# Kernel optimization log

Hardware: AMD Instinct MI355X
Metric: run time of the kernel (lower is better)

The kernel has to match this reference:

```python
import jax, jax.numpy as jnp
import numpy as np

K_N = 20          # neighbors (init kwarg k_n)
EPS = 1e-5        # BN / InstanceNorm eps (torch default)


def _conv1x1(x, w, b):
    # x: [B,C,N,K], w: [O,C], b: [O]
    return jnp.einsum('bcnk,oc->bonk', x, w) + b[None, :, None, None]


def _bn(x, g, b):
    # training-mode BatchNorm2d: stats over (B,N,K)
    mean = x.mean(axis=(0, 2, 3), keepdims=True)
    var = x.var(axis=(0, 2, 3), keepdims=True)
    return (x - mean) * jax.lax.rsqrt(var + EPS) * g[None, :, None, None] + b[None, :, None, None]


def _inorm(x):
    # InstanceNorm2d (affine=False): stats over (N,K) per (b,c)
    mean = x.mean(axis=(2, 3), keepdims=True)
    var = x.var(axis=(2, 3), keepdims=True)
    return (x - mean) * jax.lax.rsqrt(var + EPS)


def _knn(x, k):
    # x: [B,C,N] -> idx [B,N,k] of nearest neighbors (excluding self)
    sq = jnp.sum(x * x, axis=1)                                   # [B,N]
    neg_d = 2.0 * jnp.einsum('bcn,bcm->bnm', x, x) - sq[:, :, None] - sq[:, None, :]
    _, idx = jax.lax.top_k(neg_d, k + 1)
    return idx[:, :, 1:]


def _res_block(x, w1, b1, g1, be1, w2, b2, g2, be2):
    # pre=False: residual branch is identity
    out = jax.nn.relu(_bn(_inorm(_conv1x1(x, w1, b1)), g1, be1))
    out = _bn(_inorm(_conv1x1(out, w2, b2)), g2, be2)
    return jax.nn.relu(out + x)


def _forward(data, conv0_w, conv0_b, bn0_g, bn0_b, lin_w, lin_b,
             res_w1, res_b1, res_g1, res_be1, res_w2, res_b2, res_g2, res_be2):
    B, C, N = data.shape
    # graph_feature: degree feature from normalized affinity matrix
    nrm = jnp.linalg.norm(data, axis=1, keepdims=True) + 1e-5
    o = data / nrm
    A = jnp.einsum('bcn,bcm->bnm', o, o)                          # [B,N,N]
    D = (jnp.sum(A, axis=1, keepdims=True) - 1.0) / N             # [B,1,N] (subtract eye diag)
    feat = jnp.concatenate([data, jax.nn.relu(jnp.tanh(D))], axis=1)  # [B,129,N]

    idx = _knn(feat, K_N)                                         # [B,N,k]
    xt = jnp.transpose(feat, (0, 2, 1))                           # [B,N,129]
    gathered = jax.vmap(lambda xb, ib: xb[ib])(xt, idx)           # [B,N,k,129]
    center = xt[:, :, None, :]
    edge = jnp.concatenate([jnp.broadcast_to(center, gathered.shape),
                            center - gathered], axis=3)           # [B,N,k,258]
    edge = jnp.transpose(edge, (0, 3, 1, 2))                      # [B,258,N,k]

    out = jax.nn.relu(_bn(_conv1x1(edge, conv0_w, conv0_b), bn0_g, bn0_b))
    out = jnp.max(out, axis=3, keepdims=True)                     # max_pool2d (1,k) -> [B,128,N,1]
    for i in range(4):
        out = _res_block(out, res_w1[i], res_b1[i], res_g1[i], res_be1[i],
                         res_w2[i], res_b2[i], res_g2[i], res_be2[i])
    logit = _conv1x1(out, lin_w, lin_b)                           # [B,1,N,1]
    return logit.reshape(logit.shape[0], -1)                      # [B,N]


def setup_inputs() -> dict:
    B, C, N = 8, 128, 2048
    key = jax.random.key(0)
    ks = jax.random.split(key, 10)
    s = 0.05
    return {
        'data': jax.random.normal(ks[0], (B, C, N), dtype=jnp.float32),
        'x': jax.random.normal(ks[1], (B, C, N), dtype=jnp.float32),  # unused by module
        'conv0_w': jax.random.normal(ks[2], (128, 258), dtype=jnp.float32) * s,
        'conv0_b': jnp.zeros((128,), dtype=jnp.float32),
        'bn0_g': jnp.ones((128,), dtype=jnp.float32),
        'bn0_b': jnp.zeros((128,), dtype=jnp.float32),
        'lin_w': jax.random.normal(ks[3], (1, 128), dtype=jnp.float32) * s,
        'lin_b': jnp.zeros((1,), dtype=jnp.float32),
        'res_w1': jax.random.normal(ks[4], (4, 128, 128), dtype=jnp.float32) * s,
        'res_b1': jnp.zeros((4, 128), dtype=jnp.float32),
        'res_g1': jnp.ones((4, 128), dtype=jnp.float32),
        'res_be1': jnp.zeros((4, 128), dtype=jnp.float32),
        'res_w2': jax.random.normal(ks[5], (4, 128, 128), dtype=jnp.float32) * s,
        'res_b2': jnp.zeros((4, 128), dtype=jnp.float32),
        'res_g2': jnp.ones((4, 128), dtype=jnp.float32),
        'res_be2': jnp.zeros((4, 128), dtype=jnp.float32),
    }


def reference(data, x, conv0_w, conv0_b, bn0_g, bn0_b, lin_w, lin_b,
              res_w1, res_b1, res_g1, res_be1, res_w2, res_b2, res_g2, res_be2):
    # x is accepted but unused, matching the torch module
    return _forward(data, conv0_w, conv0_b, bn0_g, bn0_b, lin_w, lin_b,
                    res_w1, res_b1, res_g1, res_be1, res_w2, res_b2, res_g2, res_be2)
```

## Files before the change

kernel.cpp:

```cpp
#include <hip/hip_runtime.h>
#include <math.h>
#include <float.h>

#define NB 8
#define NC 128
#define NN 2048
#define KNN 20
#define CF 129
#define CFP 144
#define EPSV 1e-5f

#define S_OFF      0
#define BN0S_OFF   1024
#define RESST_OFF  1280
#define NRM_OFF    17664
#define ZERO_CNT   34048
#define SQN_OFF    34048
#define WCAT_OFF   50432
#define RESAFF_OFF 87552
#define FEAT_OFF   103936
#define PQ_OFF     2463232
#define X_OFF      6657536
#define SLOT_SZ    2097152
#define IDX_OFF    12948992
#define G_OFF      13276672
#define XB_OFF     46831104
#define WS_FLOATS  48928256
#define MMN_OFF    (X_OFF + SLOT_SZ)
#define MMX_OFF    (X_OFF + 2 * SLOT_SZ)

__launch_bounds__(256)
__global__ void k1a_sq(const float* __restrict__ data, float* __restrict__ ws) {
    int b = blockIdx.y;
    int n = blockIdx.x * 256 + threadIdx.x;
    int c0 = blockIdx.z * 32;
    const float* dp = data + (size_t)b * NC * NN + (size_t)c0 * NN + n;
    float acc = 0.f;
#pragma unroll
    for (int c = 0; c < 32; ++c) { float v = dp[(size_t)c * NN]; acc = fmaf(v, v, acc); }
    atomicAdd(&ws[NRM_OFF + b * NN + n], acc);
}

__launch_bounds__(256)
__global__ void k1s_colsum(const float* __restrict__ data, float* __restrict__ ws) {
    int b = blockIdx.y;
    int c0 = blockIdx.x * 16;
    int tid = threadIdx.x, w = tid >> 6, lane = tid & 63;
    __shared__ float Linv[NN];
    for (int r = tid; r < NN; r += 256)
        Linv[r] = 1.f / (sqrtf(ws[NRM_OFF + b * NN + r]) + 1e-5f);
    __syncthreads();
#pragma unroll
    for (int i = 0; i < 4; ++i) {
        int c = c0 + w * 4 + i;
        const float* dp = data + (size_t)b * NC * NN + (size_t)c * NN;
        float acc = 0.f;
        for (int n = lane; n < NN; n += 64) acc = fmaf(dp[n], Linv[n], acc);
        for (int off = 32; off; off >>= 1) acc += __shfl_down(acc, off);
        if (lane == 0) ws[S_OFF + b * NC + c] = acc;
    }
}

__launch_bounds__(256)
__global__ void k2_feat(const float* __restrict__ data, float* __restrict__ ws) {
    int b = blockIdx.y;
    int n0 = blockIdx.x * 64;
    int tid = threadIdx.x;
    __shared__ float Sb[NC];
    __shared__ __align__(16) float fT[64][CFP];
    __shared__ float redD[4][64], redQ[4][64];
    if (tid < NC) Sb[tid] = ws[S_OFF + b * NC + tid];
    __syncthreads();
    int nn = tid & 63, cg = tid >> 6;
    float dotp = 0.f, sq = 0.f;
    const float* dp = data + (size_t)b * NC * NN + n0 + nn;
    for (int c = cg; c < NC; c += 4) {
        float v = dp[(size_t)c * NN];
        fT[nn][c] = v;
        dotp += Sb[c] * v;
        sq += v * v;
    }
    redD[cg][nn] = dotp; redQ[cg][nn] = sq;
    __syncthreads();
    if (tid < 64) {
        float dt = redD[0][tid] + redD[1][tid] + redD[2][tid] + redD[3][tid];
        float sv = redQ[0][tid] + redQ[1][tid] + redQ[2][tid] + redQ[3][tid];
        float nrm = sqrtf(ws[NRM_OFF + b * NN + n0 + tid]) + 1e-5f;
        float D = (dt / nrm - 1.f) * (1.f / (float)NN);
        float f1 = tanhf(D); if (f1 < 0.f) f1 = 0.f;
        fT[tid][NC] = f1;
        for (int c = NC + 1; c < CFP; ++c) fT[tid][c] = 0.f;
        ws[SQN_OFF + b * NN + n0 + tid] = sv + f1 * f1;
    }
    __syncthreads();
    float* out = ws + FEAT_OFF + (size_t)(b * NN + n0) * CFP;
    for (int i = tid; i < 64 * CFP; i += 256) out[i] = ((float*)fT)[i];
}

__launch_bounds__(256)
__global__ void k4_wcat(const float* __restrict__ w, float* __restrict__ ws) {
    int i = blockIdx.x * 256 + threadIdx.x;
    int o = i / CFP, c = i % CFP;
    float v = 0.f;
    if (c < CF) {
        if (o < 128) v = w[o * 258 + c] + w[o * 258 + CF + c];
        else         v = w[(o - 128) * 258 + CF + c];
    }
    ws[WCAT_OFF + i] = v;
}

__launch_bounds__(256, 2)
__global__ void k3_gram(float* __restrict__ ws) {
    __shared__ __align__(16) float As[8][256];
    __shared__ __align__(16) float Bs[8][128];
    int tid = threadIdx.x;
    int b = blockIdx.z;
    int m0 = blockIdx.x * 128, n0 = blockIdx.y * 256;
    const float* F = ws + FEAT_OFF + (size_t)b * NN * CFP;
    float acc[16][8];
#pragma unroll
    for (int i = 0; i < 16; ++i)
#pragma unroll
        for (int j = 0; j < 8; ++j) acc[i][j] = 0.f;
    int rr = tid >> 1, cq = tid & 1;
    int tx = tid & 15, ty = tid >> 4;
    for (int kc = 0; kc < CFP; kc += 8) {
        float4 a0 = *(const float4*)&F[(size_t)(n0 + tid) * CFP + kc];
        float4 a1 = *(const float4*)&F[(size_t)(n0 + tid) * CFP + kc + 4];
        float4 bv = *(const float4*)&F[(size_t)(m0 + rr) * CFP + kc + cq * 4];
        __syncthreads();
        As[0][tid] = a0.x; As[1][tid] = a0.y; As[2][tid] = a0.z; As[3][tid] = a0.w;
        As[4][tid] = a1.x; As[5][tid] = a1.y; As[6][tid] = a1.z; As[7][tid] = a1.w;
        Bs[cq*4+0][rr] = bv.x; Bs[cq*4+1][rr] = bv.y; Bs[cq*4+2][rr] = bv.z; Bs[cq*4+3][rr] = bv.w;
        __syncthreads();
#pragma unroll
        for (int kk = 0; kk < 8; ++kk) {
            float a[16], bb[8];
            *(float4*)&a[0]  = *(const float4*)&As[kk][ty * 16];
            *(float4*)&a[4]  = *(const float4*)&As[kk][ty * 16 + 4];
            *(float4*)&a[8]  = *(const float4*)&As[kk][ty * 16 + 8];
            *(float4*)&a[12] = *(const float4*)&As[kk][ty * 16 + 12];
            *(float4*)&bb[0] = *(const float4*)&Bs[kk][tx * 4];
            *(float4*)&bb[4] = *(const float4*)&Bs[kk][64 + tx * 4];
#pragma unroll
            for (int i = 0; i < 16; ++i)
#pragma unroll
                for (int j = 0; j < 8; ++j) acc[i][j] = fmaf(a[i], bb[j], acc[i][j]);
        }
    }
    float sqv[8];
#pragma unroll
    for (int j = 0; j < 4; ++j) {
        sqv[j]     = ws[SQN_OFF + b * NN + m0 + tx * 4 + j];
        sqv[4 + j] = ws[SQN_OFF + b * NN + m0 + 64 + tx * 4 + j];
    }
    float* G = ws + G_OFF + (size_t)b * NN * NN;
#pragma unroll
    for (int i = 0; i < 16; ++i) {
        int row = n0 + ty * 16 + i;
        float4 o1, o2;
        o1.x = 2.f*acc[i][0]-sqv[0]; o1.y = 2.f*acc[i][1]-sqv[1];
        o1.z = 2.f*acc[i][2]-sqv[2]; o1.w = 2.f*acc[i][3]-sqv[3];
        o2.x = 2.f*acc[i][4]-sqv[4]; o2.y = 2.f*acc[i][5]-sqv[5];
        o2.z = 2.f*acc[i][6]-sqv[6]; o2.w = 2.f*acc[i][7]-sqv[7];
        *(float4*)&G[(size_t)row * NN + m0 + tx * 4]      = o1;
        *(float4*)&G[(size_t)row * NN + m0 + 64 + tx * 4] = o2;
    }
}

__launch_bounds__(256)
__global__ void ksel(float* __restrict__ ws) {
    int wid = threadIdx.x >> 6, lane = threadIdx.x & 63;
    int r = blockIdx.x * 4 + wid;
    const float* row = ws + G_OFF + (size_t)r * NN;
    float v[32];
#pragma unroll
    for (int i = 0; i < 32; ++i) v[i] = row[lane + (i << 6)];
    float b1v = -FLT_MAX, b2v = -FLT_MAX;
    int b1i = 0, b2i = 0;
#pragma unroll
    for (int i = 0; i < 32; ++i) {
        float x = v[i];
        if (x > b1v)      { b2v = b1v; b2i = b1i; b1v = x; b1i = i; }
        else if (x > b2v) { b2v = x; b2i = i; }
    }
    unsigned int mask = 0u;
    bool has2 = true;
    int* out = (int*)(ws + IDX_OFF) + (size_t)r * KNN;
    for (int k = 0; k < 21; ++k) {
        float M = b1v;
#pragma unroll
        for (int off = 1; off < 64; off <<= 1) M = fmaxf(M, __shfl_xor(M, off));
        unsigned long long tied = __ballot(b1v == M);
        int mm;
        if (__popcll(tied) > 1) {
            int cand = (b1v == M) ? ((b1i << 6) | lane) : 0x7FFFFFFF;
#pragma unroll
            for (int off = 1; off < 64; off <<= 1) {
                int oc = __shfl_xor(cand, off);
                cand = oc < cand ? oc : cand;
            }
            mm = cand;
        } else {
            int l = __ffsll(tied) - 1;
            mm = (__shfl(b1i, l) << 6) | l;
        }
        if (k > 0 && lane == 0) out[k - 1] = mm;
        if (lane == (mm & 63)) {
            mask |= 1u << b1i;
            if (has2) { b1v = b2v; b1i = b2i; has2 = false; }
            else {
                b1v = -FLT_MAX; b2v = -FLT_MAX; b1i = 0; b2i = 0;
#pragma unroll
                for (int i = 0; i < 32; ++i) {
                    float x = (mask & (1u << i)) ? -FLT_MAX : v[i];
                    if (x > b1v)      { b2v = b1v; b2i = b1i; b1v = x; b1i = i; }
                    else if (x > b2v) { b2v = x; b2i = i; }
                }
                has2 = true;
            }
        }
    }
}

__launch_bounds__(256)
__global__ void k5_pq(float* __restrict__ ws) {
    __shared__ __align__(16) float As[16][64];
    __shared__ __align__(16) float Bs[16][64];
    int tid = threadIdx.x;
    int m0 = blockIdx.x * 64, o0 = blockIdx.y * 64;
    int rr = tid >> 2, cq = tid & 3;
    int tx = tid & 15, ty = tid >> 4;
    float acc[4][4];
#pragma unroll
    for (int i = 0; i < 4; ++i)
#pragma unroll
        for (int j = 0; j < 4; ++j) acc[i][j] = 0.f;
    const float* F  = ws + FEAT_OFF;
    const float* Wc = ws + WCAT_OFF;
    for (int kc = 0; kc < CFP; kc += 16) {
        float4 av = *(const float4*)&F [(size_t)(m0 + rr) * CFP + kc + cq * 4];
        float4 bv = *(const float4*)&Wc[(size_t)(o0 + rr) * CFP + kc + cq * 4];
        __syncthreads();
        As[cq*4+0][rr]=av.x; As[cq*4+1][rr]=av.y; As[cq*4+2][rr]=av.z; As[cq*4+3][rr]=av.w;
        Bs[cq*4+0][rr]=bv.x; Bs[cq*4+1][rr]=bv.y; Bs[cq*4+2][rr]=bv.z; Bs[cq*4+3][rr]=bv.w;
        __syncthreads();
#pragma unroll
        for (int kk = 0; kk < 16; ++kk) {
            float a[4], bb[4];
            *(float4*)&a[0]  = *(const float4*)&As[kk][ty * 4];
            *(float4*)&bb[0] = *(const float4*)&Bs[kk][tx * 4];
#pragma unroll
            for (int i = 0; i < 4; ++i)
#pragma unroll
                for (int j = 0; j < 4; ++j) acc[i][j] = fmaf(a[i], bb[j], acc[i][j]);
        }
    }
#pragma unroll
    for (int i = 0; i < 4; ++i) {
        float4 o;
        o.x = acc[i][0]; o.y = acc[i][1]; o.z = acc[i][2]; o.w = acc[i][3];
        *(float4*)&ws[PQ_OFF + (size_t)(m0 + ty * 4 + i) * 256 + o0 + tx * 4] = o;
    }
}

__launch_bounds__(256)
__global__ void k6_bn0stats(float* __restrict__ ws) {
    int tid = threadIdx.x;
    int o = tid & 127, h = tid >> 7;
    int m0 = blockIdx.x * 16;
    const float* PQ = ws + PQ_OFF;
    const int* idx = (const int*)(ws + IDX_OFF);
    float* MMn = ws + MMN_OFF;
    float* MMx = ws + MMX_OFF;
    __shared__ float red[2][128];
    float s = 0.f, q = 0.f;
    for (int p = h; p < 16; p += 2) {
        int m = m0 + p;
        int bb = m >> 11;
        float pv = PQ[(size_t)m * 256 + o];
        const int* ip = idx + (size_t)m * KNN;
        float mn = FLT_MAX, mx = -FLT_MAX;
        for (int k = 0; k < KNN; ++k) {
            int j = ip[k];
            float val = pv - PQ[(size_t)(bb * NN + j) * 256 + 128 + o];
            s += val; q += val * val;
            mn = fminf(mn, val); mx = fmaxf(mx, val);
        }
        MMn[(size_t)m * NC + o] = mn;
        MMx[(size_t)m * NC + o] = mx;
    }
    red[h][o] = s; __syncthreads();
    if (tid < 128) atomicAdd(&ws[BN0S_OFF + tid], red[0][tid] + red[1][tid]);
    __syncthreads();
    red[h][o] = q; __syncthreads();
    if (tid < 128) atomicAdd(&ws[BN0S_OFF + 128 + tid], red[0][tid] + red[1][tid]);
}

__launch_bounds__(256)
__global__ void k8_apply(float* __restrict__ ws, const float* __restrict__ g,
                         const float* __restrict__ be) {
    int e = blockIdx.x * 256 + threadIdx.x;
    int fi = e * 4;
    int o = fi & 127;
    const float cnt = 1.f / (float)(NB * NN * KNN);
    float4 sum4 = *(const float4*)&ws[BN0S_OFF + o];
    float4 ssq4 = *(const float4*)&ws[BN0S_OFF + 128 + o];
    float4 g4   = *(const float4*)&g[o];
    float4 be4  = *(const float4*)&be[o];
    float4 mn = *(const float4*)&ws[MMN_OFF + fi];
    float4 mx = *(const float4*)&ws[MMX_OFF + fi];
    float4 r;
#define BN0_DO(comp) { \
    float m_ = sum4.comp * cnt; \
    float v_ = ssq4.comp * cnt - m_ * m_; if (v_ < 0.f) v_ = 0.f; \
    float sc_ = g4.comp * rsqrtf(v_ + EPSV); \
    float sh_ = be4.comp - m_ * sc_; \
    r.comp = fmaxf(fmaf(sc_ > 0.f ? mx.comp : mn.comp, sc_, sh_), 0.f); }
    BN0_DO(x) BN0_DO(y) BN0_DO(z) BN0_DO(w)
#undef BN0_DO
    *(float4*)&ws[X_OFF + fi] = r;
}

__launch_bounds__(256)
__global__ void k9f_conv(const float* __restrict__ x, const float* __restrict__ w,
                         float* __restrict__ y, float* __restrict__ stats,
                         const float* __restrict__ aff, const float* __restrict__ xin,
                         float* __restrict__ xw) {
    __shared__ __align__(16) float As[16][64];
    __shared__ __align__(16) float Bs[16][64];
    __shared__ float red[16][64];
    int tid = threadIdx.x;
    int m0 = blockIdx.x * 64, o0 = blockIdx.y * 64;
    int rr = tid >> 2, cq = tid & 3;
    int tx = tid & 15, ty = tid >> 4;
    int bA = (m0 + rr) >> 11;
    float acc[4][4];
#pragma unroll
    for (int i = 0; i < 4; ++i)
#pragma unroll
        for (int j = 0; j < 4; ++j) acc[i][j] = 0.f;
    for (int kc = 0; kc < NC; kc += 16) {
        float4 av = *(const float4*)&x[(size_t)(m0 + rr) * NC + kc + cq * 4];
        if (aff) {
            int c = kc + cq * 4;
            float4 sc4 = *(const float4*)&aff[bA * 128 + c];
            float4 sh4 = *(const float4*)&aff[1024 + bA * 128 + c];
            av.x = fmaf(av.x, sc4.x, sh4.x);
            av.y = fmaf(av.y, sc4.y, sh4.y);
            av.z = fmaf(av.z, sc4.z, sh4.z);
            av.w = fmaf(av.w, sc4.w, sh4.w);
            if (xin) {
                float4 xv = *(const float4*)&xin[(size_t)(m0 + rr) * NC + kc + cq * 4];
                av.x += xv.x; av.y += xv.y; av.z += xv.z; av.w += xv.w;
            }
            av.x = fmaxf(av.x, 0.f); av.y = fmaxf(av.y, 0.f);
            av.z = fmaxf(av.z, 0.f); av.w = fmaxf(av.w, 0.f);
            if (xw && blockIdx.y == 0)
                *(float4*)&xw[(size_t)(m0 + rr) * NC + kc + cq * 4] = av;
        }
        float4 bv = *(const float4*)&w[(size_t)(o0 + rr) * NC + kc + cq * 4];
        __syncthreads();
        As[cq*4+0][rr]=av.x; As[cq*4+1][rr]=av.y; As[cq*4+2][rr]=av.z; As[cq*4+3][rr]=av.w;
        Bs[cq*4+0][rr]=bv.x; Bs[cq*4+1][rr]=bv.y; Bs[cq*4+2][rr]=bv.z; Bs[cq*4+3][rr]=bv.w;
        __syncthreads();
#pragma unroll
        for (int kk = 0; kk < 16; ++kk) {
            float a[4], bb[4];
            *(float4*)&a[0]  = *(const float4*)&As[kk][ty * 4];
            *(float4*)&bb[0] = *(const float4*)&Bs[kk][tx * 4];
#pragma unroll
            for (int i = 0; i < 4; ++i)
#pragma unroll
                for (int j = 0; j < 4; ++j) acc[i][j] = fmaf(a[i], bb[j], acc[i][j]);
        }
    }
#pragma unroll
    for (int i = 0; i < 4; ++i) {
        float4 o;
        o.x = acc[i][0]; o.y = acc[i][1]; o.z = acc[i][2]; o.w = acc[i][3];
        *(float4*)&y[(size_t)(m0 + ty * 4 + i) * NC + o0 + tx * 4] = o;
    }
    int b = m0 >> 11;
    float s[4], q[4];
#pragma unroll
    for (int j = 0; j < 4; ++j) {
        s[j] = acc[0][j] + acc[1][j] + acc[2][j] + acc[3][j];
        q[j] = acc[0][j]*acc[0][j] + acc[1][j]*acc[1][j] + acc[2][j]*acc[2][j] + acc[3][j]*acc[3][j];
    }
    *(float4*)&red[ty][tx * 4] = make_float4(s[0], s[1], s[2], s[3]);
    __syncthreads();
    if (tid < 64) {
        float t = 0.f;
#pragma unroll
        for (int g2 = 0; g2 < 16; ++g2) t += red[g2][tid];
        atomicAdd(&stats[b * NC + o0 + tid], t);
    }
    __syncthreads();
    *(float4*)&red[ty][tx * 4] = make_float4(q[0], q[1], q[2], q[3]);
    __syncthreads();
    if (tid < 64) {
        float t = 0.f;
#pragma unroll
        for (int g2 = 0; g2 < 16; ++g2) t += red[g2][tid];
        atomicAdd(&stats[1024 + b * NC + o0 + tid], t);
    }
}

__launch_bounds__(1024)
__global__ void k10_fin(float* __restrict__ ws, int L, const float* __restrict__ g,
                        const float* __restrict__ be) {
    __shared__ float vv[1024];
    __shared__ float rsbn[128];
    int tid = threadIdx.x;
    const float* st = ws + RESST_OFF + L * 2048;
    float sum = st[tid], ssq = st[1024 + tid];
    float m = sum * (1.f / (float)NN);
    float v = ssq * (1.f / (float)NN) - m * m; if (v < 0.f) v = 0.f;
    float r = rsqrtf(v + EPSV);
    vv[tid] = v / (v + EPSV);
    __syncthreads();
    if (tid < 128) {
        float a = 0.f;
        for (int bb = 0; bb < NB; ++bb) a += vv[bb * 128 + tid];
        rsbn[tid] = rsqrtf(a * (1.f / (float)NB) + EPSV);
    }
    __syncthreads();
    int o = tid & 127;
    float sc = r * rsbn[o] * g[o];
    float sh = be[o] - m * sc;
    float* aff = ws + RESAFF_OFF + L * 2048;
    aff[tid] = sc; aff[1024 + tid] = sh;
}

__launch_bounds__(256)
__global__ void k12_logit(const float* __restrict__ y2, const float* __restrict__ xin,
                          const float* __restrict__ aff, const float* __restrict__ lw,
                          const float* __restrict__ lb, float* __restrict__ out) {
    __shared__ float w[128];
    int tid = threadIdx.x;
    if (tid < 128) w[tid] = lw[tid];
    __syncthreads();
    int m = blockIdx.x * 256 + tid;
    int b = m >> 11;
    const float* yp = y2 + (size_t)m * NC;
    const float* xp = xin + (size_t)m * NC;
    const float* sc = aff + b * 128;
    const float* sh = aff + 1024 + b * 128;
    float acc = lb[0];
    for (int c = 0; c < NC; c += 4) {
        float4 yv = *(const float4*)&yp[c];
        float4 xv = *(const float4*)&xp[c];
        float v0 = fmaxf(fmaf(yv.x, sc[c],     sh[c])     + xv.x, 0.f);
        float v1 = fmaxf(fmaf(yv.y, sc[c + 1], sh[c + 1]) + xv.y, 0.f);
        float v2 = fmaxf(fmaf(yv.z, sc[c + 2], sh[c + 2]) + xv.z, 0.f);
        float v3 = fmaxf(fmaf(yv.w, sc[c + 3], sh[c + 3]) + xv.w, 0.f);
        acc += v0 * w[c] + v1 * w[c + 1] + v2 * w[c + 2] + v3 * w[c + 3];
    }
    out[m] = acc;
}

extern "C" void kernel_launch(void* const* d_in, const int* in_sizes, int n_in,
                              void* d_out, int out_size, void* d_ws, size_t ws_size,
                              hipStream_t stream) {
    if (ws_size < (size_t)WS_FLOATS * 4) return;
    const float* data    = (const float*)d_in[0];
    const float* conv0_w = (const float*)d_in[2];
    const float* bn0_g   = (const float*)d_in[4];
    const float* bn0_b   = (const float*)d_in[5];
    const float* lin_w   = (const float*)d_in[6];
    const float* lin_b   = (const float*)d_in[7];
    const float* res_w1  = (const float*)d_in[8];
    const float* res_g1  = (const float*)d_in[10];
    const float* res_be1 = (const float*)d_in[11];
    const float* res_w2  = (const float*)d_in[12];
    const float* res_g2  = (const float*)d_in[14];
    const float* res_be2 = (const float*)d_in[15];
    float* ws  = (float*)d_ws;
    float* out = (float*)d_out;

    hipMemsetAsync(d_ws, 0, ZERO_CNT * sizeof(float), stream);
    k1a_sq<<<dim3(8, 8, 4), 256, 0, stream>>>(data, ws);
    k1s_colsum<<<dim3(8, 8), 256, 0, stream>>>(data, ws);
    k2_feat<<<dim3(32, 8), 256, 0, stream>>>(data, ws);
    k4_wcat<<<144, 256, 0, stream>>>(conv0_w, ws);
    k3_gram<<<dim3(16, 8, 8), 256, 0, stream>>>(ws);
    ksel<<<4096, 256, 0, stream>>>(ws);
    k5_pq<<<dim3(256, 4), 256, 0, stream>>>(ws);
    k6_bn0stats<<<1024, 256, 0, stream>>>(ws);
    k8_apply<<<2048, 256, 0, stream>>>(ws, bn0_g, bn0_b);

    float* XA = ws + X_OFF;
    float* Y1 = ws + X_OFF + SLOT_SZ;
    float* Y2 = ws + X_OFF + 2 * SLOT_SZ;
    float* XB = ws + XB_OFF;

    k9f_conv<<<dim3(256, 2), 256, 0, stream>>>(XA, res_w1, Y1, ws + RESST_OFF, nullptr, nullptr, nullptr);
    k10_fin<<<1, 1024, 0, stream>>>(ws, 0, res_g1, res_be1);
    k9f_conv<<<dim3(256, 2), 256, 0, stream>>>(Y1, res_w2, Y2, ws + RESST_OFF + 2048,
                                               ws + RESAFF_OFF, nullptr, nullptr);
    k10_fin<<<1, 1024, 0, stream>>>(ws, 1, res_g2, res_be2);
    float* xcur = XA; float* xnext = XB;
    for (int i = 1; i < 4; ++i) {
        int L = 2 * i, L2 = 2 * i + 1;
        k9f_conv<<<dim3(256, 2), 256, 0, stream>>>(Y2, res_w1 + i * 16384, Y1,
                                                   ws + RESST_OFF + L * 2048,
                                                   ws + RESAFF_OFF + (L - 1) * 2048, xcur, xnext);
        k10_fin<<<1, 1024, 0, stream>>>(ws, L, res_g1 + i * 128, res_be1 + i * 128);
        k9f_conv<<<dim3(256, 2), 256, 0, stream>>>(Y1, res_w2 + i * 16384, Y2,
                                                   ws + RESST_OFF + L2 * 2048,
                                                   ws + RESAFF_OFF + L * 2048, nullptr, nullptr);
        k10_fin<<<1, 1024, 0, stream>>>(ws, L2, res_g2 + i * 128, res_be2 + i * 128);
        float* t = xcur; xcur = xnext; xnext = t;
    }
    k12_logit<<<64, 256, 0, stream>>>(Y2, xcur, ws + RESAFF_OFF + 7 * 2048, lin_w, lin_b, out);
}
```

Before: 445.2 us.

## Double-buffer gram kernel shared tiles with 128x128 blocks and prefetch

```diff
diff --git a/kernel.cpp b/kernel.cpp
--- a/kernel.cpp
+++ b/kernel.cpp
@@ -109,45 +109,65 @@
     ws[WCAT_OFF + i] = v;
 }
 
-__launch_bounds__(256, 2)
+__launch_bounds__(256)
 __global__ void k3_gram(float* __restrict__ ws) {
-    __shared__ __align__(16) float As[8][256];
-    __shared__ __align__(16) float Bs[8][128];
+    __shared__ __align__(16) float As[2][16][128];
+    __shared__ __align__(16) float Bs[2][16][128];
     int tid = threadIdx.x;
     int b = blockIdx.z;
-    int m0 = blockIdx.x * 128, n0 = blockIdx.y * 256;
+    int m0 = blockIdx.x * 128, n0 = blockIdx.y * 128;
     const float* F = ws + FEAT_OFF + (size_t)b * NN * CFP;
-    float acc[16][8];
-#pragma unroll
-    for (int i = 0; i < 16; ++i)
+    int rr = tid >> 1, hh = tid & 1;
+    int tx = tid & 15, ty = tid >> 4;
+    float acc[8][8];
+#pragma unroll
+    for (int i = 0; i < 8; ++i)
 #pragma unroll
         for (int j = 0; j < 8; ++j) acc[i][j] = 0.f;
-    int rr = tid >> 1, cq = tid & 1;
-    int tx = tid & 15, ty = tid >> 4;
-    for (int kc = 0; kc < CFP; kc += 8) {
-        float4 a0 = *(const float4*)&F[(size_t)(n0 + tid) * CFP + kc];
-        float4 a1 = *(const float4*)&F[(size_t)(n0 + tid) * CFP + kc + 4];
-        float4 bv = *(const float4*)&F[(size_t)(m0 + rr) * CFP + kc + cq * 4];
-        __syncthreads();
-        As[0][tid] = a0.x; As[1][tid] = a0.y; As[2][tid] = a0.z; As[3][tid] = a0.w;
-        As[4][tid] = a1.x; As[5][tid] = a1.y; As[6][tid] = a1.z; As[7][tid] = a1.w;
-        Bs[cq*4+0][rr] = bv.x; Bs[cq*4+1][rr] = bv.y; Bs[cq*4+2][rr] = bv.z; Bs[cq*4+3][rr] = bv.w;
-        __syncthreads();
-#pragma unroll
-        for (int kk = 0; kk < 8; ++kk) {
-            float a[16], bb[8];
-            *(float4*)&a[0]  = *(const float4*)&As[kk][ty * 16];
-            *(float4*)&a[4]  = *(const float4*)&As[kk][ty * 16 + 4];
-            *(float4*)&a[8]  = *(const float4*)&As[kk][ty * 16 + 8];
-            *(float4*)&a[12] = *(const float4*)&As[kk][ty * 16 + 12];
-            *(float4*)&bb[0] = *(const float4*)&Bs[kk][tx * 4];
-            *(float4*)&bb[4] = *(const float4*)&Bs[kk][64 + tx * 4];
-#pragma unroll
-            for (int i = 0; i < 16; ++i)
+
+    const float* Arow = &F[(size_t)(n0 + rr) * CFP + hh * 8];
+    const float* Brow = &F[(size_t)(m0 + rr) * CFP + hh * 8];
+    float4 ra0 = *(const float4*)&Arow[0];
+    float4 ra1 = *(const float4*)&Arow[4];
+    float4 rb0 = *(const float4*)&Brow[0];
+    float4 rb1 = *(const float4*)&Brow[4];
+    int kbase = hh * 8;
+#define STAGE(buf) { \
+    As[buf][kbase+0][rr]=ra0.x; As[buf][kbase+1][rr]=ra0.y; As[buf][kbase+2][rr]=ra0.z; As[buf][kbase+3][rr]=ra0.w; \
+    As[buf][kbase+4][rr]=ra1.x; As[buf][kbase+5][rr]=ra1.y; As[buf][kbase+6][rr]=ra1.z; As[buf][kbase+7][rr]=ra1.w; \
+    Bs[buf][kbase+0][rr]=rb0.x; Bs[buf][kbase+1][rr]=rb0.y; Bs[buf][kbase+2][rr]=rb0.z; Bs[buf][kbase+3][rr]=rb0.w; \
+    Bs[buf][kbase+4][rr]=rb1.x; Bs[buf][kbase+5][rr]=rb1.y; Bs[buf][kbase+6][rr]=rb1.z; Bs[buf][kbase+7][rr]=rb1.w; }
+    STAGE(0);
+    __syncthreads();
+    int cur = 0;
+    for (int t = 0; t < 9; ++t) {
+        if (t < 8) {
+            int kc = (t + 1) * 16;
+            ra0 = *(const float4*)&Arow[kc];
+            ra1 = *(const float4*)&Arow[kc + 4];
+            rb0 = *(const float4*)&Brow[kc];
+            rb1 = *(const float4*)&Brow[kc + 4];
+        }
+#pragma unroll
+        for (int kk = 0; kk < 16; ++kk) {
+            float a[8], bb[8];
+            *(float4*)&a[0]  = *(const float4*)&As[cur][kk][ty * 8];
+            *(float4*)&a[4]  = *(const float4*)&As[cur][kk][ty * 8 + 4];
+            *(float4*)&bb[0] = *(const float4*)&Bs[cur][kk][tx * 4];
+            *(float4*)&bb[4] = *(const float4*)&Bs[cur][kk][64 + tx * 4];
+#pragma unroll
+            for (int i = 0; i < 8; ++i)
 #pragma unroll
                 for (int j = 0; j < 8; ++j) acc[i][j] = fmaf(a[i], bb[j], acc[i][j]);
         }
-    }
+        if (t < 8) {
+            int nxt = cur ^ 1;
+            STAGE(nxt);
+            __syncthreads();
+            cur = nxt;
+        }
+    }
+#undef STAGE
     float sqv[8];
 #pragma unroll
     for (int j = 0; j < 4; ++j) {
@@ -156,8 +176,8 @@
     }
     float* G = ws + G_OFF + (size_t)b * NN * NN;
 #pragma unroll
-    for (int i = 0; i < 16; ++i) {
-        int row = n0 + ty * 16 + i;
+    for (int i = 0; i < 8; ++i) {
+        int row = n0 + ty * 8 + i;
         float4 o1, o2;
         o1.x = 2.f*acc[i][0]-sqv[0]; o1.y = 2.f*acc[i][1]-sqv[1];
         o1.z = 2.f*acc[i][2]-sqv[2]; o1.w = 2.f*acc[i][3]-sqv[3];
@@ -484,7 +504,7 @@
     k1s_colsum<<<dim3(8, 8), 256, 0, stream>>>(data, ws);
     k2_feat<<<dim3(32, 8), 256, 0, stream>>>(data, ws);
     k4_wcat<<<144, 256, 0, stream>>>(conv0_w, ws);
-    k3_gram<<<dim3(16, 8, 8), 256, 0, stream>>>(ws);
+    k3_gram<<<dim3(16, 16, 8), 256, 0, stream>>>(ws);
     ksel<<<4096, 256, 0, stream>>>(ws);
     k5_pq<<<dim3(256, 4), 256, 0, stream>>>(ws);
     k6_bn0stats<<<1024, 256, 0, stream>>>(ws);
```

Result: slower. 487.2 us (+9.4%).

## Fold norm-finalize into conv prologue and shrink gram tile to 128x128

Applied to the files above, without the earlier changes.

```diff
diff --git a/kernel.cpp b/kernel.cpp
--- a/kernel.cpp
+++ b/kernel.cpp
@@ -17,7 +17,6 @@
 #define ZERO_CNT   34048
 #define SQN_OFF    34048
 #define WCAT_OFF   50432
-#define RESAFF_OFF 87552
 #define FEAT_OFF   103936
 #define PQ_OFF     2463232
 #define X_OFF      6657536
@@ -109,41 +108,37 @@
     ws[WCAT_OFF + i] = v;
 }
 
-__launch_bounds__(256, 2)
+__launch_bounds__(256)
 __global__ void k3_gram(float* __restrict__ ws) {
-    __shared__ __align__(16) float As[8][256];
+    __shared__ __align__(16) float As[8][128];
     __shared__ __align__(16) float Bs[8][128];
     int tid = threadIdx.x;
     int b = blockIdx.z;
-    int m0 = blockIdx.x * 128, n0 = blockIdx.y * 256;
+    int m0 = blockIdx.x * 128, n0 = blockIdx.y * 128;
     const float* F = ws + FEAT_OFF + (size_t)b * NN * CFP;
-    float acc[16][8];
-#pragma unroll
-    for (int i = 0; i < 16; ++i)
+    float acc[8][8];
+#pragma unroll
+    for (int i = 0; i < 8; ++i)
 #pragma unroll
         for (int j = 0; j < 8; ++j) acc[i][j] = 0.f;
     int rr = tid >> 1, cq = tid & 1;
     int tx = tid & 15, ty = tid >> 4;
     for (int kc = 0; kc < CFP; kc += 8) {
-        float4 a0 = *(const float4*)&F[(size_t)(n0 + tid) * CFP + kc];
-        float4 a1 = *(const float4*)&F[(size_t)(n0 + tid) * CFP + kc + 4];
+        float4 av = *(const float4*)&F[(size_t)(n0 + rr) * CFP + kc + cq * 4];
         float4 bv = *(const float4*)&F[(size_t)(m0 + rr) * CFP + kc + cq * 4];
         __syncthreads();
-        As[0][tid] = a0.x; As[1][tid] = a0.y; As[2][tid] = a0.z; As[3][tid] = a0.w;
-        As[4][tid] = a1.x; As[5][tid] = a1.y; As[6][tid] = a1.z; As[7][tid] = a1.w;
+        As[cq*4+0][rr] = av.x; As[cq*4+1][rr] = av.y; As[cq*4+2][rr] = av.z; As[cq*4+3][rr] = av.w;
         Bs[cq*4+0][rr] = bv.x; Bs[cq*4+1][rr] = bv.y; Bs[cq*4+2][rr] = bv.z; Bs[cq*4+3][rr] = bv.w;
         __syncthreads();
 #pragma unroll
         for (int kk = 0; kk < 8; ++kk) {
-            float a[16], bb[8];
-            *(float4*)&a[0]  = *(const float4*)&As[kk][ty * 16];
-            *(float4*)&a[4]  = *(const float4*)&As[kk][ty * 16 + 4];
-            *(float4*)&a[8]  = *(const float4*)&As[kk][ty * 16 + 8];
-            *(float4*)&a[12] = *(const float4*)&As[kk][ty * 16 + 12];
+            float a[8], bb[8];
+            *(float4*)&a[0]  = *(const float4*)&As[kk][ty * 8];
+            *(float4*)&a[4]  = *(const float4*)&As[kk][ty * 8 + 4];
             *(float4*)&bb[0] = *(const float4*)&Bs[kk][tx * 4];
             *(float4*)&bb[4] = *(const float4*)&Bs[kk][64 + tx * 4];
 #pragma unroll
-            for (int i = 0; i < 16; ++i)
+            for (int i = 0; i < 8; ++i)
 #pragma unroll
                 for (int j = 0; j < 8; ++j) acc[i][j] = fmaf(a[i], bb[j], acc[i][j]);
         }
@@ -156,8 +151,8 @@
     }
     float* G = ws + G_OFF + (size_t)b * NN * NN;
 #pragma unroll
-    for (int i = 0; i < 16; ++i) {
-        int row = n0 + ty * 16 + i;
+    for (int i = 0; i < 8; ++i) {
+        int row = n0 + ty * 8 + i;
         float4 o1, o2;
         o1.x = 2.f*acc[i][0]-sqv[0]; o1.y = 2.f*acc[i][1]-sqv[1];
         o1.z = 2.f*acc[i][2]-sqv[2]; o1.w = 2.f*acc[i][3]-sqv[3];
@@ -325,16 +320,41 @@
 __launch_bounds__(256)
 __global__ void k9f_conv(const float* __restrict__ x, const float* __restrict__ w,
                          float* __restrict__ y, float* __restrict__ stats,
-                         const float* __restrict__ aff, const float* __restrict__ xin,
-                         float* __restrict__ xw) {
+                         const float* __restrict__ statsIn,
+                         const float* __restrict__ g, const float* __restrict__ be,
+                         const float* __restrict__ xin, float* __restrict__ xw) {
     __shared__ __align__(16) float As[16][64];
     __shared__ __align__(16) float Bs[16][64];
     __shared__ float red[16][64];
+    __shared__ float vvv[8][128];
+    __shared__ float scs[128], shs[128];
     int tid = threadIdx.x;
     int m0 = blockIdx.x * 64, o0 = blockIdx.y * 64;
+    int bA = m0 >> 11;
+    if (statsIn) {
+        for (int e = tid; e < 1024; e += 256) {
+            float sum = statsIn[e], ssq = statsIn[1024 + e];
+            float m_ = sum * (1.f / (float)NN);
+            float v_ = ssq * (1.f / (float)NN) - m_ * m_; if (v_ < 0.f) v_ = 0.f;
+            vvv[e >> 7][e & 127] = v_ / (v_ + EPSV);
+        }
+        __syncthreads();
+        if (tid < 128) {
+            float a = 0.f;
+#pragma unroll
+            for (int b2 = 0; b2 < NB; ++b2) a += vvv[b2][tid];
+            float rsbn = rsqrtf(a * (1.f / (float)NB) + EPSV);
+            float sum = statsIn[bA * 128 + tid], ssq = statsIn[1024 + bA * 128 + tid];
+            float m_ = sum * (1.f / (float)NN);
+            float v_ = ssq * (1.f / (float)NN) - m_ * m_; if (v_ < 0.f) v_ = 0.f;
+            float sc_ = rsqrtf(v_ + EPSV) * rsbn * g[tid];
+            scs[tid] = sc_;
+            shs[tid] = be[tid] - m_ * sc_;
+        }
+        __syncthreads();
+    }
     int rr = tid >> 2, cq = tid & 3;
     int tx = tid & 15, ty = tid >> 4;
-    int bA = (m0 + rr) >> 11;
     float acc[4][4];
 #pragma unroll
     for (int i = 0; i < 4; ++i)
@@ -342,14 +362,12 @@
         for (int j = 0; j < 4; ++j) acc[i][j] = 0.f;
     for (int kc = 0; kc < NC; kc += 16) {
         float4 av = *(const float4*)&x[(size_t)(m0 + rr) * NC + kc + cq * 4];
-        if (aff) {
+        if (statsIn) {
             int c = kc + cq * 4;
-            float4 sc4 = *(const float4*)&aff[bA * 128 + c];
-            float4 sh4 = *(const float4*)&aff[1024 + bA * 128 + c];
-            av.x = fmaf(av.x, sc4.x, sh4.x);
-            av.y = fmaf(av.y, sc4.y, sh4.y);
-            av.z = fmaf(av.z, sc4.z, sh4.z);
-            av.w = fmaf(av.w, sc4.w, sh4.w);
+            av.x = fmaf(av.x, scs[c],     shs[c]);
+            av.y = fmaf(av.y, scs[c + 1], shs[c + 1]);
+            av.z = fmaf(av.z, scs[c + 2], shs[c + 2]);
+            av.w = fmaf(av.w, scs[c + 3], shs[c + 3]);
             if (xin) {
                 float4 xv = *(const float4*)&xin[(size_t)(m0 + rr) * NC + kc + cq * 4];
                 av.x += xv.x; av.y += xv.y; av.z += xv.z; av.w += xv.w;
@@ -381,7 +399,6 @@
         o.x = acc[i][0]; o.y = acc[i][1]; o.z = acc[i][2]; o.w = acc[i][3];
         *(float4*)&y[(size_t)(m0 + ty * 4 + i) * NC + o0 + tx * 4] = o;
     }
-    int b = m0 >> 11;
     float s[4], q[4];
 #pragma unroll
     for (int j = 0; j < 4; ++j) {
@@ -394,7 +411,7 @@
         float t = 0.f;
 #pragma unroll
         for (int g2 = 0; g2 < 16; ++g2) t += red[g2][tid];
-        atomicAdd(&stats[b * NC + o0 + tid], t);
+        atomicAdd(&stats[bA * NC + o0 + tid], t);
     }
     __syncthreads();
     *(float4*)&red[ty][tx * 4] = make_float4(q[0], q[1], q[2], q[3]);
@@ -403,59 +420,54 @@
         float t = 0.f;
 #pragma unroll
         for (int g2 = 0; g2 < 16; ++g2) t += red[g2][tid];
-        atomicAdd(&stats[1024 + b * NC + o0 + tid], t);
-    }
-}
-
-__launch_bounds__(1024)
-__global__ void k10_fin(float* __restrict__ ws, int L, const float* __restrict__ g,
-                        const float* __restrict__ be) {
-    __shared__ float vv[1024];
-    __shared__ float rsbn[128];
+        atomicAdd(&stats[1024 + bA * NC + o0 + tid], t);
+    }
+}
+
+__launch_bounds__(256)
+__global__ void k12_logit(const float* __restrict__ y2, const float* __restrict__ xin,
+                          const float* __restrict__ statsIn,
+                          const float* __restrict__ g, const float* __restrict__ be,
+                          const float* __restrict__ lw, const float* __restrict__ lb,
+                          float* __restrict__ out) {
+    __shared__ float wsh[128];
+    __shared__ float vvv[8][128];
+    __shared__ float scs[128], shs[128];
     int tid = threadIdx.x;
-    const float* st = ws + RESST_OFF + L * 2048;
-    float sum = st[tid], ssq = st[1024 + tid];
-    float m = sum * (1.f / (float)NN);
-    float v = ssq * (1.f / (float)NN) - m * m; if (v < 0.f) v = 0.f;
-    float r = rsqrtf(v + EPSV);
-    vv[tid] = v / (v + EPSV);
+    int b = (blockIdx.x * 256) >> 11;
+    if (tid < 128) wsh[tid] = lw[tid];
+    for (int e = tid; e < 1024; e += 256) {
+        float sum = statsIn[e], ssq = statsIn[1024 + e];
+        float m_ = sum * (1.f / (float)NN);
+        float v_ = ssq * (1.f / (float)NN) - m_ * m_; if (v_ < 0.f) v_ = 0.f;
+        vvv[e >> 7][e & 127] = v_ / (v_ + EPSV);
+    }
     __syncthreads();
     if (tid < 128) {
         float a = 0.f;
-        for (int bb = 0; bb < NB; ++bb) a += vv[bb * 128 + tid];
-        rsbn[tid] = rsqrtf(a * (1.f / (float)NB) + EPSV);
-    }
-    __syncthreads();
-    int o = tid & 127;
-    float sc = r * rsbn[o] * g[o];
-    float sh = be[o] - m * sc;
-    float* aff = ws + RESAFF_OFF + L * 2048;
-    aff[tid] = sc; aff[1024 + tid] = sh;
-}
-
-__launch_bounds__(256)
-__global__ void k12_logit(const float* __restrict__ y2, const float* __restrict__ xin,
-                          const float* __restrict__ aff, const float* __restrict__ lw,
-                          const float* __restrict__ lb, float* __restrict__ out) {
-    __shared__ float w[128];
-    int tid = threadIdx.x;
-    if (tid < 128) w[tid] = lw[tid];
+#pragma unroll
+        for (int b2 = 0; b2 < NB; ++b2) a += vvv[b2][tid];
+        float rsbn = rsqrtf(a * (1.f / (float)NB) + EPSV);
+        float sum = statsIn[b * 128 + tid], ssq = statsIn[1024 + b * 128 + tid];
+        float m_ = sum * (1.f / (float)NN);
+        float v_ = ssq * (1.f / (float)NN) - m_ * m_; if (v_ < 0.f) v_ = 0.f;
+        float sc_ = rsqrtf(v_ + EPSV) * rsbn * g[tid];
+        scs[tid] = sc_;
+        shs[tid] = be[tid] - m_ * sc_;
+    }
     __syncthreads();
     int m = blockIdx.x * 256 + tid;
-    int b = m >> 11;
     const float* yp = y2 + (size_t)m * NC;
     const float* xp = xin + (size_t)m * NC;
-    const float* sc = aff + b * 128;
-    const float* sh = aff + 1024 + b * 128;
     float acc = lb[0];
     for (int c = 0; c < NC; c += 4) {
         float4 yv = *(const float4*)&yp[c];
         float4 xv = *(const float4*)&xp[c];
-        float v0 = fmaxf(fmaf(yv.x, sc[c],     sh[c])     + xv.x, 0.f);
-        float v1 = fmaxf(fmaf(yv.y, sc[c + 1], sh[c + 1]) + xv.y, 0.f);
-        float v2 = fmaxf(fmaf(yv.z, sc[c + 2], sh[c + 2]) + xv.z, 0.f);
-        float v3 = fmaxf(fmaf(yv.w, sc[c + 3], sh[c + 3]) + xv.w, 0.f);
-        acc += v0 * w[c] + v1 * w[c + 1] + v2 * w[c + 2] + v3 * w[c + 3];
+        float v0 = fmaxf(fmaf(yv.x, scs[c],     shs[c])     + xv.x, 0.f);
+        float v1 = fmaxf(fmaf(yv.y, scs[c + 1], shs[c + 1]) + xv.y, 0.f);
+        float v2 = fmaxf(fmaf(yv.z, scs[c + 2], shs[c + 2]) + xv.z, 0.f);
+        float v3 = fmaxf(fmaf(yv.w, scs[c + 3], shs[c + 3]) + xv.w, 0.f);
+        acc += v0 * wsh[c] + v1 * wsh[c + 1] + v2 * wsh[c + 2] + v3 * wsh[c + 3];
     }
     out[m] = acc;
 }
@@ -484,7 +496,7 @@
     k1s_colsum<<<dim3(8, 8), 256, 0, stream>>>(data, ws);
     k2_feat<<<dim3(32, 8), 256, 0, stream>>>(data, ws);
     k4_wcat<<<144, 256, 0, stream>>>(conv0_w, ws);
-    k3_gram<<<dim3(16, 8, 8), 256, 0, stream>>>(ws);
+    k3_gram<<<dim3(16, 16, 8), 256, 0, stream>>>(ws);
     ksel<<<4096, 256, 0, stream>>>(ws);
     k5_pq<<<dim3(256, 4), 256, 0, stream>>>(ws);
     k6_bn0stats<<<1024, 256, 0, stream>>>(ws);
@@ -494,24 +506,25 @@
     float* Y1 = ws + X_OFF + SLOT_SZ;
     float* Y2 = ws + X_OFF + 2 * SLOT_SZ;
     float* XB = ws + XB_OFF;
-
-    k9f_conv<<<dim3(256, 2), 256, 0, stream>>>(XA, res_w1, Y1, ws + RESST_OFF, nullptr, nullptr, nullptr);
-    k10_fin<<<1, 1024, 0, stream>>>(ws, 0, res_g1, res_be1);
-    k9f_conv<<<dim3(256, 2), 256, 0, stream>>>(Y1, res_w2, Y2, ws + RESST_OFF + 2048,
-                                               ws + RESAFF_OFF, nullptr, nullptr);
-    k10_fin<<<1, 1024, 0, stream>>>(ws, 1, res_g2, res_be2);
+    float* ST = ws + RESST_OFF;
+
+    k9f_conv<<<dim3(256, 2), 256, 0, stream>>>(XA, res_w1, Y1, ST,
+                                               nullptr, nullptr, nullptr, nullptr, nullptr);
+    k9f_conv<<<dim3(256, 2), 256, 0, stream>>>(Y1, res_w2, Y2, ST + 2048,
+                                               ST, res_g1, res_be1, nullptr, nullptr);
     float* xcur = XA; float* xnext = XB;
     for (int i = 1; i < 4; ++i) {
         int L = 2 * i, L2 = 2 * i + 1;
-        k9f_conv<<<dim3(256, 2), 256, 0, stream>>>(Y2, res_w1 + i * 16384, Y1,
-                                                   ws + RESST_OFF + L * 2048,
-                                                   ws + RESAFF_OFF + (L - 1) * 2048, xcur, xnext);
-        k10_fin<<<1, 1024, 0, stream>>>(ws, L, res_g1 + i * 128, res_be1 + i * 128);
-        k9f_conv<<<dim3(256, 2), 256, 0, stream>>>(Y1, res_w2 + i * 16384, Y2,
-                                                   ws + RESST_OFF + L2 * 2048,
-                                                   ws + RESAFF_OFF + L * 2048, nullptr, nullptr);
-        k10_fin<<<1, 1024, 0, stream>>>(ws, L2, res_g2 + i * 128, res_be2 + i * 128);
+        k9f_conv<<<dim3(256, 2), 256, 0, stream>>>(Y2, res_w1 + i * 16384, Y1, ST + L * 2048,
+                                                   ST + (L - 1) * 2048,
+                                                   res_g2 + (i - 1) * 128, res_be2 + (i - 1) * 128,
+                                                   xcur, xnext);
+        k9f_conv<<<dim3(256, 2), 256, 0, stream>>>(Y1, res_w2 + i * 16384, Y2, ST + L2 * 2048,
+                                                   ST + L * 2048,
+                                                   res_g1 + i * 128, res_be1 + i * 128,
+                                                   nullptr, nullptr);
         float* t = xcur; xcur = xnext; xnext = t;
     }
-    k12_logit<<<64, 256, 0, stream>>>(Y2, xcur, ws + RESAFF_OFF + 7 * 2048, lin_w, lin_b, out);
-}
+    k12_logit<<<64, 256, 0, stream>>>(Y2, xcur, ST + 7 * 2048, res_g2 + 3 * 128, res_be2 + 3 * 128,
+                                      lin_w, lin_b, out);
+}
```

Result: no change. 441.0 us (-0.9%).
